# Optimization experiments

Measured on AMD Instinct MI355X. Metric: run time of the kernel, lower is better.

The kernel has to match this reference:

```python
import jax, jax.numpy as jnp
import numpy as np

N = 100000   # nodes
E = 1600000  # edges
G = 64       # graphs in batch
DIMS = [(7, 128), (128, 128), (128, 256)]
EPS = 1e-5


def setup_inputs() -> dict:
    key = jax.random.key(0)
    ks = jax.random.split(key, 32)
    inp = {}
    inp["x"] = jax.random.normal(ks[0], (N, 7), dtype=jnp.float32)
    inp["edge_index"] = jax.random.randint(ks[1], (2, E), 0, N, dtype=jnp.int64)
    inp["batch"] = jnp.sort(jax.random.randint(ks[2], (N,), 0, G, dtype=jnp.int64))
    ki = 3
    for i, (din, dout) in enumerate(DIMS):
        inp[f"Wl{i}"] = jax.random.normal(ks[ki], (din, dout), dtype=jnp.float32) * 0.05; ki += 1
        inp[f"bl{i}"] = jnp.zeros((dout,), dtype=jnp.float32)
        inp[f"Wr{i}"] = jax.random.normal(ks[ki], (din, dout), dtype=jnp.float32) * 0.05; ki += 1
        inp[f"g{i}"] = jax.random.uniform(ks[ki], (dout,), dtype=jnp.float32) + 0.5; ki += 1
        inp[f"be{i}"] = jax.random.normal(ks[ki], (dout,), dtype=jnp.float32) * 0.1; ki += 1
        inp[f"rm{i}"] = jax.random.normal(ks[ki], (dout,), dtype=jnp.float32) * 0.1; ki += 1
        inp[f"rv{i}"] = jax.random.uniform(ks[ki], (dout,), dtype=jnp.float32) + 0.5; ki += 1
    return inp


def _sage(x, src, dst, Wl, bl, Wr):
    # mean-aggregate neighbor features: out[i] = mean_{(j->i)} x[j]
    agg = jax.ops.segment_sum(x[src], dst, num_segments=N)          # [N, din]
    cnt = jax.ops.segment_sum(jnp.ones((src.shape[0],), x.dtype), dst, num_segments=N)
    mean = agg / jnp.maximum(cnt, 1.0)[:, None]
    return x @ Wl + bl + mean @ Wr


def _bn_relu(x, g, be, rm, rv):
    # BatchNorm1d in eval mode (running stats) + ReLU; dropout is a no-op in eval
    return jax.nn.relu((x - rm) * jax.lax.rsqrt(rv + EPS) * g + be)


def reference(x, edge_index, batch,
              Wl0, bl0, Wr0, g0, be0, rm0, rv0,
              Wl1, bl1, Wr1, g1, be1, rm1, rv1,
              Wl2, bl2, Wr2, g2, be2, rm2, rv2):
    src, dst = edge_index[0], edge_index[1]
    layers = [(Wl0, bl0, Wr0, g0, be0, rm0, rv0),
              (Wl1, bl1, Wr1, g1, be1, rm1, rv1),
              (Wl2, bl2, Wr2, g2, be2, rm2, rv2)]
    for Wl, bl, Wr, g, be, rm, rv in layers:
        x = _sage(x, src, dst, Wl, bl, Wr)
        x = _bn_relu(x, g, be, rm, rv)
    pooled = jax.ops.segment_sum(x, batch, num_segments=G)  # global_add_pool
    return (pooled, x)
```

## Files before the change

### kernel.cpp

```cpp
#include <hip/hip_runtime.h>
#include <hip/hip_bf16.h>

#define EPSV 1e-5f
#define PSHIFT 6
#define PMASK 63
#define PCAP 1536
#define B1SHIFT 11
#define B1MASK ((1 << B1SHIFT) - 1)
#define B1CAP 34816
#define SPLIT 16

typedef __attribute__((ext_vector_type(8))) short bf16x8;
typedef __attribute__((ext_vector_type(4))) float f32x4;
typedef __attribute__((ext_vector_type(4))) unsigned u32x4;

__device__ __forceinline__ float bf2f(unsigned short u) {
    unsigned x = ((unsigned)u) << 16;
    return __builtin_bit_cast(float, x);
}
__device__ __forceinline__ unsigned short f2bf(float f) {
    unsigned x = __builtin_bit_cast(unsigned, f);
    unsigned r = (x + 0x7fffu + ((x >> 16) & 1u)) >> 16;
    return (unsigned short)r;
}
__device__ __forceinline__ f32x4 bflo4(u32x4 v) {
    f32x4 r;
    r.x = __builtin_bit_cast(float, v.x << 16);
    r.y = __builtin_bit_cast(float, v.y << 16);
    r.z = __builtin_bit_cast(float, v.z << 16);
    r.w = __builtin_bit_cast(float, v.w << 16);
    return r;
}
__device__ __forceinline__ f32x4 bfhi4(u32x4 v) {
    f32x4 r;
    r.x = __builtin_bit_cast(float, v.x & 0xffff0000u);
    r.y = __builtin_bit_cast(float, v.y & 0xffff0000u);
    r.z = __builtin_bit_cast(float, v.z & 0xffff0000u);
    r.w = __builtin_bit_cast(float, v.w & 0xffff0000u);
    return r;
}


__global__ __launch_bounds__(256) void k_scatter1(const int* __restrict__ src,
                                                  const int* __restrict__ dst,
                                                  int* __restrict__ bcnt1,
                                                  unsigned* __restrict__ stg1,
                                                  int E, int NB1) {
    __shared__ int hist[64], sbase[64], scur[64];
    int t = threadIdx.x;
    int base = blockIdx.x * 2048;
    if (t < 64) { hist[t] = 0; scur[t] = 0; }
    __syncthreads();
    unsigned val[8];
    int cb[8];
#pragma unroll
    for (int k = 0; k < 8; k++) {
        int i = base + k * 256 + t;
        if (i < E) {
            int d = __builtin_nontemporal_load(&dst[i]);
            int s = __builtin_nontemporal_load(&src[i]);
            cb[k] = d >> B1SHIFT;
            val[k] = ((unsigned)s << B1SHIFT) | (unsigned)(d & B1MASK);
            atomicAdd(&hist[cb[k]], 1);
        } else
            cb[k] = -1;
    }
    __syncthreads();
    if (t < NB1 && hist[t] > 0) sbase[t] = atomicAdd(&bcnt1[t], hist[t]);
    __syncthreads();
#pragma unroll
    for (int k = 0; k < 8; k++) {
        if (cb[k] >= 0) {
            int r = atomicAdd(&scur[cb[k]], 1);
            int slot = sbase[cb[k]] + r;
            if (slot < B1CAP) stg1[(size_t)cb[k] * B1CAP + slot] = val[k];
        }
    }
}

__global__ __launch_bounds__(256) void k_scatter2(const int* __restrict__ bcnt1,
                                                  const unsigned* __restrict__ stg1,
                                                  int* __restrict__ pcnt,
                                                  unsigned* __restrict__ pstg) {
    __shared__ int hist[32], sbase[32], scur[32];
    int cb = blockIdx.x >> 4;
    int sl = blockIdx.x & (SPLIT - 1);
    int t = threadIdx.x;
    if (t < 32) { hist[t] = 0; scur[t] = 0; }
    int cnt = min(bcnt1[cb], B1CAP);
    int per = (cnt + SPLIT - 1) / SPLIT;
    int lo = sl * per, hi = min(lo + per, cnt);
    __syncthreads();
    const unsigned* sp = stg1 + (size_t)cb * B1CAP;
    for (int j = lo + t; j < hi; j += 256)
        atomicAdd(&hist[(sp[j] >> 6) & 31], 1);
    __syncthreads();
    if (t < 32 && hist[t] > 0) sbase[t] = atomicAdd(&pcnt[(cb << 5) + t], hist[t]);
    __syncthreads();
    for (int j = lo + t; j < hi; j += 256) {
        unsigned v = sp[j];
        int pr = (v >> 6) & 31;
        int r = atomicAdd(&scur[pr], 1);
        int slot = sbase[pr] + r;
        if (slot < PCAP)
            pstg[(size_t)((cb << 5) + pr) * PCAP + slot] =
                ((v >> 5) & ~63u) | (v & 63u);
    }
}

__global__ __launch_bounds__(256) void k_meta(const int* __restrict__ pcnt,
                                              int* __restrict__ pbase,
                                              int* __restrict__ off,
                                              const int* __restrict__ batch,
                                              int* __restrict__ gstart,
                                              int NPART, int Nn, int G) {
    if (blockIdx.x == 1) {
        int g = threadIdx.x;
        if (g > G) return;
        if (g == G) {
            gstart[G] = Nn;
            return;
        }
        int lo = 0, hi = Nn;
        while (lo < hi) {
            int mid = (lo + hi) >> 1;
            if (batch[mid] < g) lo = mid + 1;
            else hi = mid;
        }
        gstart[g] = lo;
        return;
    }
    __shared__ int red[256];
    int t = threadIdx.x;
    int chunk = (NPART + 255) / 256;
    int lo = t * chunk, hi = min(lo + chunk, NPART);
    int s = 0;
    for (int p = lo; p < hi; p++) {
        int tt = min(pcnt[p], PCAP);
        pbase[p] = tt;
        s += tt;
    }
    red[t] = s;
    __syncthreads();
    for (int d = 1; d < 256; d <<= 1) {
        int v = (t >= d) ? red[t - d] : 0;
        __syncthreads();
        red[t] += v;
        __syncthreads();
    }
    int base = (t == 0) ? 0 : red[t - 1];
    for (int p = lo; p < hi; p++) {
        int tt = pbase[p];
        pbase[p] = base;
        base += tt;
    }
    if (t == 255) off[Nn] = red[255];
}

__global__ __launch_bounds__(256) void k_build(const int* __restrict__ pcnt,
                                               const unsigned* __restrict__ pstg,
                                               const int* __restrict__ pbase,
                                               int* __restrict__ off,
                                               int* __restrict__ csr, int Nn) {
    __shared__ unsigned ed[PCAP];
    __shared__ int srt[PCAP];
    __shared__ int cnt[64], loff[64], cur[64];
    int p = blockIdx.x, t = threadIdx.x;
    int tot = min(pcnt[p], PCAP);
    if (t < 64) cnt[t] = 0;
    __syncthreads();
    const unsigned* sp = pstg + (size_t)p * PCAP;
    for (int j = t; j < tot; j += 256) {
        unsigned e = __builtin_nontemporal_load(&sp[j]);
        ed[j] = e;
        atomicAdd(&cnt[e & PMASK], 1);
    }
    __syncthreads();
    if (t == 0) {
        int a = 0;
        for (int j = 0; j < 64; j++) {
            loff[j] = a;
            cur[j] = a;
            a += cnt[j];
        }
    }
    __syncthreads();
    int base = pbase[p];
    int node0 = p << PSHIFT;
    if (t < 64 && node0 + t < Nn) off[node0 + t] = base + loff[t];
    for (int j = t; j < tot; j += 256) {
        unsigned e = ed[j];
        int pos = atomicAdd(&cur[e & PMASK], 1);
        srt[pos] = (int)(e >> PSHIFT);
    }
    __syncthreads();
    for (int j = t; j < tot; j += 256) csr[base + j] = srt[j];
}


__global__ __launch_bounds__(256) void k_agg7(const float* __restrict__ x,
                                              const int* __restrict__ off,
                                              const int* __restrict__ csr,
                                              float* __restrict__ mean, int n) {
    int i = (blockIdx.x * 256 + threadIdx.x) >> 3;
    int r = threadIdx.x & 7;
    if (i >= n) return;
    int a = off[i], b = off[i + 1];
    float acc = 0.f;
    if (r < 7) {
        int j = a;
        for (; j + 1 < b; j += 2)
            acc += x[(size_t)csr[j] * 7 + r] + x[(size_t)csr[j + 1] * 7 + r];
        if (j < b) acc += x[(size_t)csr[j] * 7 + r];
    }
    float inv = 1.0f / (float)max(b - a, 1);
    if (r < 7) mean[(size_t)i * 7 + r] = acc * inv;
}

__global__ __launch_bounds__(256) void k_agg128(const unsigned short* __restrict__ x,
                                                const int* __restrict__ off,
                                                const int* __restrict__ csr,
                                                unsigned short* __restrict__ mean,
                                                int n) {
    int q = (blockIdx.x * 256 + threadIdx.x) >> 4;
    int sl = threadIdx.x & 15;
    if (q >= n) return;
    int a = off[q], b = off[q + 1];
    const u32x4* xr = (const u32x4*)x;
    f32x4 aL = {0.f, 0.f, 0.f, 0.f}, aH = {0.f, 0.f, 0.f, 0.f};
    int j = a;
    for (; j + 3 < b; j += 4) {
        int s0 = csr[j], s1 = csr[j + 1], s2 = csr[j + 2], s3 = csr[j + 3];
        u32x4 v0 = xr[(size_t)s0 * 16 + sl];
        u32x4 v1 = xr[(size_t)s1 * 16 + sl];
        u32x4 v2 = xr[(size_t)s2 * 16 + sl];
        u32x4 v3 = xr[(size_t)s3 * 16 + sl];
        aL += bflo4(v0) + bflo4(v1) + bflo4(v2) + bflo4(v3);
        aH += bfhi4(v0) + bfhi4(v1) + bfhi4(v2) + bfhi4(v3);
    }
    for (; j < b; j++) {
        u32x4 v = xr[(size_t)csr[j] * 16 + sl];
        aL += bflo4(v);
        aH += bfhi4(v);
    }
    float inv = 1.0f / (float)max(b - a, 1);
    u32x4 o;
    o.x = (unsigned)f2bf(aL.x * inv) | ((unsigned)f2bf(aH.x * inv) << 16);
    o.y = (unsigned)f2bf(aL.y * inv) | ((unsigned)f2bf(aH.y * inv) << 16);
    o.z = (unsigned)f2bf(aL.z * inv) | ((unsigned)f2bf(aH.z * inv) << 16);
    o.w = (unsigned)f2bf(aL.w * inv) | ((unsigned)f2bf(aH.w * inv) << 16);
    __builtin_nontemporal_store(o, (u32x4*)mean + (size_t)q * 16 + sl);
}


__global__ __launch_bounds__(256) void k_prepw_all(
    const float* __restrict__ Wl1, const float* __restrict__ Wr1,
    const float* __restrict__ Wl2, const float* __restrict__ Wr2,
    unsigned short* __restrict__ Wlt1, unsigned short* __restrict__ Wrt1,
    unsigned short* __restrict__ Wlt2, unsigned short* __restrict__ Wrt2) {
    int u = blockIdx.x * 256 + threadIdx.x;
    const float* W;
    unsigned short* Wt;
    int Ncols, v;
    if (u < 32768) {
        v = u & 16383;
        W = (u < 16384) ? Wl1 : Wr1;
        Wt = (u < 16384) ? Wlt1 : Wrt1;
        Ncols = 128;
    } else {
        v = (u - 32768) & 32767;
        W = (u < 65536) ? Wl2 : Wr2;
        Wt = (u < 65536) ? Wlt2 : Wrt2;
        Ncols = 256;
    }
    int n = v % Ncols, k = v / Ncols;
    Wt[(size_t)n * 128 + k] = f2bf(W[(size_t)k * Ncols + n]);
}


__global__ __launch_bounds__(256) void k_layer0(
    const float* __restrict__ x, const float* __restrict__ mean,
    const float* __restrict__ Wl, const float* __restrict__ bl,
    const float* __restrict__ Wr, const float* __restrict__ g,
    const float* __restrict__ be, const float* __restrict__ rm,
    const float* __restrict__ rv, unsigned short* __restrict__ out, int n) {
    int tid = threadIdx.x;
    int col = tid & 127;
    int r = tid >> 7;
    int row = blockIdx.x * 2 + r;
    if (row >= n) return;
    float sc = g[col] * rsqrtf(rv[col] + EPSV);
    float sh = (bl[col] - rm[col]) * sc + be[col];
    const float* xp = x + (size_t)row * 7;
    const float* mp = mean + (size_t)row * 7;
    float acc = 0.f;
#pragma unroll
    for (int k = 0; k < 7; k++) acc += xp[k] * Wl[k * 128 + col];
#pragma unroll
    for (int k = 0; k < 7; k++) acc += mp[k] * Wr[k * 128 + col];
    float h = acc * sc + sh;
    out[(size_t)row * 128 + col] = f2bf(fmaxf(h, 0.f));
}


template <int COLS, int DOUT, bool BF16OUT>
__global__ __launch_bounds__(256) void k_mfma_layer(
    const unsigned short* __restrict__ xin, const unsigned short* __restrict__ meanb,
    const unsigned short* __restrict__ Wlt, const unsigned short* __restrict__ Wrt,
    const float* __restrict__ bl, const float* __restrict__ g,
    const float* __restrict__ be, const float* __restrict__ rm,
    const float* __restrict__ rv, void* __restrict__ outv,
    const int* __restrict__ batchp, float* __restrict__ pooled, int n) {
    __shared__ unsigned short As[64 * 40];
    __shared__ unsigned short Bs[COLS * 40];
    __shared__ float plds[COLS];

    int tid = threadIdx.x;
    int wave = tid >> 6;
    int lane = tid & 63;
    int m = lane & 15;
    int half = lane >> 4;
    int row0 = blockIdx.x * 64;
    int colbase = blockIdx.y * COLS;

    if (!BF16OUT && tid < COLS) plds[tid] = 0.f;

    const int NCB = COLS / 16;
    f32x4 acc[NCB] = {};

    for (int s = 0; s < 8; s++) {
        int pass = s >> 2;
        int k0 = (s & 3) * 32;
        const unsigned short* Asrc = pass ? meanb : xin;
        const unsigned short* Wt = pass ? Wrt : Wlt;

        __syncthreads();
        {
            int rr = tid >> 2;
            int ks = (tid & 3) * 8;
            int grow = row0 + rr;
            float4 v = make_float4(0.f, 0.f, 0.f, 0.f);
            if (grow < n) v = *(const float4*)&Asrc[(size_t)grow * 128 + k0 + ks];
            *(float4*)&As[rr * 40 + ks] = v;
        }
#pragma unroll
        for (int rep = 0; rep < COLS / 64; rep++) {
            int u = tid + rep * 256;
            int nn = u >> 2;
            int ks = (u & 3) * 8;
            float4 v = *(const float4*)&Wt[(size_t)(colbase + nn) * 128 + k0 + ks];
            *(float4*)&Bs[nn * 40 + ks] = v;
        }
        __syncthreads();

        bf16x8 a = *(const bf16x8*)&As[(wave * 16 + m) * 40 + half * 8];
#pragma unroll
        for (int cb = 0; cb < NCB; cb++) {
            bf16x8 b = *(const bf16x8*)&Bs[(cb * 16 + m) * 40 + half * 8];
            acc[cb] = __builtin_amdgcn_mfma_f32_16x16x32_bf16(a, b, acc[cb], 0, 0, 0);
        }
    }

    bool uni = true;
    int gmin = 0;
    if (!BF16OUT) {
        int last = min(row0 + 63, n - 1);
        gmin = batchp[row0];
        uni = (gmin == batchp[last]);
    }

    float* outf = (float*)outv;
    unsigned short* outb = (unsigned short*)outv;
    float colsum[NCB];
#pragma unroll
    for (int cb = 0; cb < NCB; cb++) colsum[cb] = 0.f;

#pragma unroll
    for (int cb = 0; cb < NCB; cb++) {
        int col = colbase + cb * 16 + m;
        float sc = g[col] * rsqrtf(rv[col] + EPSV);
        float sh = (bl[col] - rm[col]) * sc + be[col];
#pragma unroll
        for (int reg = 0; reg < 4; reg++) {
            int r0 = row0 + wave * 16 + half * 4 + reg;
            if (r0 < n) {
                float h = fmaxf(acc[cb][reg] * sc + sh, 0.f);
                if (BF16OUT) {
                    outb[(size_t)r0 * DOUT + col] = f2bf(h);
                } else {
                    outf[(size_t)r0 * DOUT + col] = h;
                    if (uni) colsum[cb] += h;
                    else atomicAdd(&pooled[(size_t)batchp[r0] * 256 + col], h);
                }
            }
        }
    }

    if (!BF16OUT) {
        if (uni) {
#pragma unroll
            for (int cb = 0; cb < NCB; cb++) atomicAdd(&plds[cb * 16 + m], colsum[cb]);
            __syncthreads();
            if (tid < COLS)
                atomicAdd(&pooled[(size_t)gmin * 256 + colbase + tid], plds[tid]);
        }
    }
}


extern "C" void kernel_launch(void* const* d_in, const int* in_sizes, int n_in,
                              void* d_out, int out_size, void* d_ws, size_t ws_size,
                              hipStream_t stream) {
    const float* x = (const float*)d_in[0];
    const int* ei = (const int*)d_in[1];
    const int* batch = (const int*)d_in[2];
    const int N = in_sizes[0] / 7;
    const int E = in_sizes[1] / 2;
    const int G = 64;
    const int* src = ei;
    const int* dst = ei + E;
    const int NPART = (N + PMASK) >> PSHIFT;
    const int NB1 = (N + (1 << B1SHIFT) - 1) >> B1SHIFT;

    const float* P[21];
    for (int i = 0; i < 21; i++) P[i] = (const float*)d_in[3 + i];
    const float **L0 = P, **L1 = P + 7, **L2 = P + 14;

    char* w = (char*)d_ws;
    auto carve = [&](size_t bytes) {
        void* p = (void*)w;
        w += (bytes + 255) & ~(size_t)255;
        return p;
    };
    int* cnts = (int*)carve((size_t)(64 + NPART) * 4);
    int* bcnt1 = cnts;
    int* pcnt = cnts + 64;
    unsigned* stg1 = (unsigned*)carve((size_t)NB1 * B1CAP * 4);
    unsigned* pstg = (unsigned*)carve((size_t)NPART * PCAP * 4);
    int* pbase = (int*)carve((size_t)NPART * 4);
    int* off = (int*)carve(((size_t)N + 1) * 4);
    int* gstart = (int*)carve(((size_t)G + 1) * 4);
    float* mean7 = (float*)carve((size_t)N * 7 * 4);
    unsigned short* x1 = (unsigned short*)carve((size_t)N * 128 * 2);
    unsigned short* meanb = (unsigned short*)carve((size_t)N * 128 * 2);
    unsigned short* Wlt1 = (unsigned short*)carve((size_t)128 * 128 * 2);
    unsigned short* Wrt1 = (unsigned short*)carve((size_t)128 * 128 * 2);
    unsigned short* Wlt2 = (unsigned short*)carve((size_t)128 * 256 * 2);
    unsigned short* Wrt2 = (unsigned short*)carve((size_t)128 * 256 * 2);
    int* csr = (int*)stg1;

    float* pooled = (float*)d_out;
    float* x3 = (float*)d_out + (size_t)G * 256;

    hipMemsetAsync(cnts, 0, (size_t)(64 + NPART) * 4, stream);
    hipMemsetAsync(pooled, 0, (size_t)G * 256 * 4, stream);

    k_scatter1<<<(E + 2047) / 2048, 256, 0, stream>>>(src, dst, bcnt1, stg1, E, NB1);
    k_scatter2<<<NB1 * SPLIT, 256, 0, stream>>>(bcnt1, stg1, pcnt, pstg);
    k_meta<<<2, 256, 0, stream>>>(pcnt, pbase, off, batch, gstart, NPART, N, G);
    k_build<<<NPART, 256, 0, stream>>>(pcnt, pstg, pbase, off, csr, N);
    k_prepw_all<<<(98304 + 255) / 256, 256, 0, stream>>>(L1[0], L1[2], L2[0], L2[2],
                                                         Wlt1, Wrt1, Wlt2, Wrt2);

    k_agg7<<<(N * 8 + 255) / 256, 256, 0, stream>>>(x, off, csr, mean7, N);
    k_layer0<<<(N + 1) / 2, 256, 0, stream>>>(x, mean7, L0[0], L0[1], L0[2], L0[3],
                                              L0[4], L0[5], L0[6], x1, N);

    k_agg128<<<((size_t)N * 16 + 255) / 256, 256, 0, stream>>>(x1, off, csr, meanb, N);
    k_mfma_layer<128, 128, true><<<dim3((N + 63) / 64, 1), 256, 0, stream>>>(
        x1, meanb, Wlt1, Wrt1, L1[1], L1[3], L1[4], L1[5], L1[6], x1, nullptr,
        nullptr, N);

    k_agg128<<<((size_t)N * 16 + 255) / 256, 256, 0, stream>>>(x1, off, csr, meanb, N);
    k_mfma_layer<128, 256, false><<<dim3((N + 63) / 64, 2), 256, 0, stream>>>(
        x1, meanb, Wlt2, Wrt2, L2[1], L2[3], L2[4], L2[5], L2[6], x3, batch,
        pooled, N);
}
```

Measured before the change: 510.6 us.

## Unroll gather to 8 edges and move pooling into separate kernel

The neighbor-mean gather kernel now issues up to eight row loads per step and reads CSR indices with nontemporal loads, to get more memory loads in flight. Its output store becomes a normal cached store, presumably so the following GEMM layer finds meanb in cache. The global add pool is taken out of the final MFMA layer epilogue and done by a new k_pool kernel that re-reads x3 per graph and sums its columns. This removes atomics and the batch checks from the GEMM, at the cost of one extra launch and a second pass over the 100000x256 fp32 output.

New measurement: 490.9 us. -3.9%, faster.

```diff
diff --git a/kernel.cpp b/kernel.cpp
--- a/kernel.cpp
+++ b/kernel.cpp
@@ -229,17 +229,35 @@
     const u32x4* xr = (const u32x4*)x;
     f32x4 aL = {0.f, 0.f, 0.f, 0.f}, aH = {0.f, 0.f, 0.f, 0.f};
     int j = a;
+    for (; j + 7 < b; j += 8) {
+        u32x4 v[8];
+#pragma unroll
+        for (int t = 0; t < 8; t++) {
+            int s = __builtin_nontemporal_load(&csr[j + t]);
+            v[t] = xr[(size_t)s * 16 + sl];
+        }
+#pragma unroll
+        for (int t = 0; t < 8; t++) {
+            aL += bflo4(v[t]);
+            aH += bfhi4(v[t]);
+        }
+    }
     for (; j + 3 < b; j += 4) {
-        int s0 = csr[j], s1 = csr[j + 1], s2 = csr[j + 2], s3 = csr[j + 3];
-        u32x4 v0 = xr[(size_t)s0 * 16 + sl];
-        u32x4 v1 = xr[(size_t)s1 * 16 + sl];
-        u32x4 v2 = xr[(size_t)s2 * 16 + sl];
-        u32x4 v3 = xr[(size_t)s3 * 16 + sl];
-        aL += bflo4(v0) + bflo4(v1) + bflo4(v2) + bflo4(v3);
-        aH += bfhi4(v0) + bfhi4(v1) + bfhi4(v2) + bfhi4(v3);
+        u32x4 v[4];
+#pragma unroll
+        for (int t = 0; t < 4; t++) {
+            int s = __builtin_nontemporal_load(&csr[j + t]);
+            v[t] = xr[(size_t)s * 16 + sl];
+        }
+#pragma unroll
+        for (int t = 0; t < 4; t++) {
+            aL += bflo4(v[t]);
+            aH += bfhi4(v[t]);
+        }
     }
     for (; j < b; j++) {
-        u32x4 v = xr[(size_t)csr[j] * 16 + sl];
+        int s = __builtin_nontemporal_load(&csr[j]);
+        u32x4 v = xr[(size_t)s * 16 + sl];
         aL += bflo4(v);
         aH += bfhi4(v);
     }
@@ -249,7 +267,7 @@
     o.y = (unsigned)f2bf(aL.y * inv) | ((unsigned)f2bf(aH.y * inv) << 16);
     o.z = (unsigned)f2bf(aL.z * inv) | ((unsigned)f2bf(aH.z * inv) << 16);
     o.w = (unsigned)f2bf(aL.w * inv) | ((unsigned)f2bf(aH.w * inv) << 16);
-    __builtin_nontemporal_store(o, (u32x4*)mean + (size_t)q * 16 + sl);
+    *((u32x4*)mean + (size_t)q * 16 + sl) = o;
 }
 
 
@@ -309,11 +327,9 @@
     const unsigned short* __restrict__ Wlt, const unsigned short* __restrict__ Wrt,
     const float* __restrict__ bl, const float* __restrict__ g,
     const float* __restrict__ be, const float* __restrict__ rm,
-    const float* __restrict__ rv, void* __restrict__ outv,
-    const int* __restrict__ batchp, float* __restrict__ pooled, int n) {
+    const float* __restrict__ rv, void* __restrict__ outv, int n) {
     __shared__ unsigned short As[64 * 40];
     __shared__ unsigned short Bs[COLS * 40];
-    __shared__ float plds[COLS];
 
     int tid = threadIdx.x;
     int wave = tid >> 6;
@@ -322,8 +338,6 @@
     int half = lane >> 4;
     int row0 = blockIdx.x * 64;
     int colbase = blockIdx.y * COLS;
-
-    if (!BF16OUT && tid < COLS) plds[tid] = 0.f;
 
     const int NCB = COLS / 16;
     f32x4 acc[NCB] = {};
@@ -361,20 +375,8 @@
         }
     }
 
-    bool uni = true;
-    int gmin = 0;
-    if (!BF16OUT) {
-        int last = min(row0 + 63, n - 1);
-        gmin = batchp[row0];
-        uni = (gmin == batchp[last]);
-    }
-
     float* outf = (float*)outv;
     unsigned short* outb = (unsigned short*)outv;
-    float colsum[NCB];
-#pragma unroll
-    for (int cb = 0; cb < NCB; cb++) colsum[cb] = 0.f;
-
 #pragma unroll
     for (int cb = 0; cb < NCB; cb++) {
         int col = colbase + cb * 16 + m;
@@ -385,26 +387,25 @@
             int r0 = row0 + wave * 16 + half * 4 + reg;
             if (r0 < n) {
                 float h = fmaxf(acc[cb][reg] * sc + sh, 0.f);
-                if (BF16OUT) {
-                    outb[(size_t)r0 * DOUT + col] = f2bf(h);
-                } else {
-                    outf[(size_t)r0 * DOUT + col] = h;
-                    if (uni) colsum[cb] += h;
-                    else atomicAdd(&pooled[(size_t)batchp[r0] * 256 + col], h);
-                }
+                if (BF16OUT) outb[(size_t)r0 * DOUT + col] = f2bf(h);
+                else outf[(size_t)r0 * DOUT + col] = h;
             }
         }
     }
-
-    if (!BF16OUT) {
-        if (uni) {
-#pragma unroll
-            for (int cb = 0; cb < NCB; cb++) atomicAdd(&plds[cb * 16 + m], colsum[cb]);
-            __syncthreads();
-            if (tid < COLS)
-                atomicAdd(&pooled[(size_t)gmin * 256 + colbase + tid], plds[tid]);
-        }
-    }
+}
+
+
+__global__ __launch_bounds__(256) void k_pool(const float* __restrict__ x3,
+                                              const int* __restrict__ gstart,
+                                              float* __restrict__ pooled, int G) {
+    const int S = 16;
+    int g = blockIdx.x / S;
+    int s = blockIdx.x % S;
+    int a = gstart[g], b = gstart[g + 1];
+    int col = threadIdx.x;
+    float acc = 0.f;
+    for (int r = a + s; r < b; r += S) acc += x3[(size_t)r * 256 + col];
+    atomicAdd(&pooled[g * 256 + col], acc);
 }
 
 
@@ -468,11 +469,11 @@
 
     k_agg128<<<((size_t)N * 16 + 255) / 256, 256, 0, stream>>>(x1, off, csr, meanb, N);
     k_mfma_layer<128, 128, true><<<dim3((N + 63) / 64, 1), 256, 0, stream>>>(
-        x1, meanb, Wlt1, Wrt1, L1[1], L1[3], L1[4], L1[5], L1[6], x1, nullptr,
-        nullptr, N);
+        x1, meanb, Wlt1, Wrt1, L1[1], L1[3], L1[4], L1[5], L1[6], x1, N);
 
     k_agg128<<<((size_t)N * 16 + 255) / 256, 256, 0, stream>>>(x1, off, csr, meanb, N);
     k_mfma_layer<128, 256, false><<<dim3((N + 63) / 64, 2), 256, 0, stream>>>(
-        x1, meanb, Wlt2, Wrt2, L2[1], L2[3], L2[4], L2[5], L2[6], x3, batch,
-        pooled, N);
-}
+        x1, meanb, Wlt2, Wrt2, L2[1], L2[3], L2[4], L2[5], L2[6], x3, N);
+
+    k_pool<<<G * 16, 256, 0, stream>>>(x3, gstart, pooled, G);
+}
```
